# Kernel optimization log

Measured on AMD Instinct MI355X. Metric: run time of the kernel, lower is better.

The kernel has to match this reference:

```python
import jax, jax.numpy as jnp
import numpy as np

B, N, DIN, D, NH, NL = 4, 256, 4, 64, 4, 2
DH = D // NH
EPS = 1e-5
SLOPE = 0.01  # torch LeakyReLU default negative_slope


def setup_inputs() -> dict:
    key = jax.random.key(0)
    ks = jax.random.split(key, 16)
    def p(k, shape, s=0.05):
        return jax.random.normal(k, shape, jnp.float32) * s
    return {
        "feature": jax.random.normal(ks[0], (B, N, N, DIN), jnp.float32),
        "W1": p(ks[1], (DIN, D)), "b1": jnp.zeros((D,), jnp.float32),
        "mw": p(ks[2], (NH, D)), "mb": jnp.zeros((NH,), jnp.float32),
        "bn_gamma": jnp.ones((D,), jnp.float32), "bn_beta": jnp.zeros((D,), jnp.float32),
        "Wq": p(ks[3], (NL, D, D)), "bq": jnp.zeros((NL, D), jnp.float32),
        "Wk": p(ks[4], (NL, D, D)), "bk": jnp.zeros((NL, D), jnp.float32),
        "Wv": p(ks[5], (NL, D, D)), "bv": jnp.zeros((NL, D), jnp.float32),
        "Wo": p(ks[6], (NL, D, D)), "bo": jnp.zeros((NL, D), jnp.float32),
        "ln1_g": jnp.ones((NL, D), jnp.float32), "ln1_b": jnp.zeros((NL, D), jnp.float32),
        "Wff1": p(ks[7], (NL, D, 2 * D)), "bff1": jnp.zeros((NL, 2 * D), jnp.float32),
        "Wff2": p(ks[8], (NL, 2 * D, D)), "bff2": jnp.zeros((NL, D), jnp.float32),
        "ln2_g": jnp.ones((NL, D), jnp.float32), "ln2_b": jnp.zeros((NL, D), jnp.float32),
    }


def _leaky(x):
    return jnp.where(x >= 0, x, SLOPE * x)


def _layer_norm(x, g, b):
    m = x.mean(axis=-1, keepdims=True)
    v = x.var(axis=-1, keepdims=True)
    return g * (x - m) / jnp.sqrt(v + EPS) + b


def reference(feature, W1, b1, mw, mb, bn_gamma, bn_beta,
              Wq, bq, Wk, bk, Wv, bv, Wo, bo, ln1_g, ln1_b,
              Wff1, bff1, Wff2, bff2, ln2_g, ln2_b):
    # linear1: (B,N,N,DIN) -> (B,N,N,D)
    feat = feature @ W1 + b1
    # per-head scalar attention score over node pairs: (NH,B,N,N)
    s = jnp.einsum('bijh,nh->nbij', feat, mw) + mb[:, None, None, None]
    w = jnp.exp(_leaky(s))
    w = w / w.sum(axis=3, keepdims=True)  # softmax-like over second node dim j
    # weighted aggregation: sum over i, then mean over heads -> (B,N,D)
    h = jnp.einsum('nbij,bijh->bjh', w, feat) / NH
    # BatchNorm1d over channels D, stats over (B,N) (training-mode, biased var)
    m = h.mean(axis=(0, 1))
    v = h.var(axis=(0, 1))
    x = bn_gamma * (h - m) / jnp.sqrt(v + EPS) + bn_beta  # (B,N,D)
    # standard post-LN TransformerEncoder, NL layers
    scale = 1.0 / np.sqrt(DH).astype(np.float32)
    for l in range(NL):
        q = (x @ Wq[l] + bq[l]).reshape(B, N, NH, DH)
        k = (x @ Wk[l] + bk[l]).reshape(B, N, NH, DH)
        vv = (x @ Wv[l] + bv[l]).reshape(B, N, NH, DH)
        a = jax.nn.softmax(jnp.einsum('bqhd,bkhd->bhqk', q, k) * scale, axis=-1)
        o = jnp.einsum('bhqk,bkhd->bqhd', a, vv).reshape(B, N, D) @ Wo[l] + bo[l]
        x = _layer_norm(x + o, ln1_g[l], ln1_b[l])
        f = jax.nn.relu(x @ Wff1[l] + bff1[l]) @ Wff2[l] + bff2[l]
        x = _layer_norm(x + f, ln2_g[l], ln2_b[l])
    return x
```

## Files before the change

### kernel.cpp

```cpp
#include <hip/hip_runtime.h>
#include <math.h>

#define B 4
#define N 256
#define DIN 4
#define D 64
#define NH 4
#define NL 2
#define DH 16

constexpr float EPS = 1e-5f;
constexpr float SLOPE = 0.01f;

__global__ void __launch_bounds__(512) k_rowsum(
    const float* __restrict__ feature, const float* __restrict__ W1,
    const float* __restrict__ b1, const float* __restrict__ mw,
    const float* __restrict__ mb, float* __restrict__ rs,
    float* __restrict__ bnacc ) {
    __shared__ float M[16];
    __shared__ float C[4];
    __shared__ float part[32];
    int t = threadIdx.x;
    int lane = t & 63, w = t >> 6;
    int cb = blockIdx.x;
    if (cb == 0 && t < 128) bnacc[t] = 0.f;
    if (t < 16) {
        int n = t >> 2, kk = t & 3;
        float s = 0.f;
        for (int d = 0; d < D; ++d) s += W1[kk * D + d] * mw[n * D + d];
        M[t] = s;
    } else if (t < 20) {
        int n = t - 16;
        float s = mb[n];
        for (int d = 0; d < D; ++d) s += b1[d] * mw[n * D + d];
        C[n] = s;
    }
    __syncthreads();

    int r = w & 3, mh = w >> 2;
    int bi = cb * 4 + r;
    const float4* fb = (const float4*)(feature) + (size_t)bi * N;
    float sn[4] = {0.f, 0.f, 0.f, 0.f};
#pragma unroll
    for (int mm = 0; mm < 2; ++mm) {
        float4 f = fb[lane + 64 * (mh * 2 + mm)];
#pragma unroll
        for (int n = 0; n < 4; ++n) {
            float s = C[n] + f.x * M[n*4+0] + f.y * M[n*4+1] + f.z * M[n*4+2] + f.w * M[n*4+3];
            s = (s >= 0.f) ? s : SLOPE * s;
            sn[n] += __expf(s);
        }
    }
#pragma unroll
    for (int n = 0; n < 4; ++n)
#pragma unroll
        for (int off = 32; off > 0; off >>= 1) sn[n] += __shfl_xor(sn[n], off);
    if (lane == 0) {
#pragma unroll
        for (int n = 0; n < 4; ++n) part[w * 4 + n] = sn[n];
    }
    __syncthreads();
    if (t < 16) {
        int rr = t >> 2, n = t & 3;
        rs[((size_t)(cb * 4 + rr)) * 4 + n] = part[rr * 4 + n] + part[(rr + 4) * 4 + n];
    }
}

__global__ void __launch_bounds__(512) k_aggregate(
    const float* __restrict__ feature, const float* __restrict__ W1,
    const float* __restrict__ b1, const float* __restrict__ mw,
    const float* __restrict__ mb, const float* __restrict__ rs,
    float* __restrict__ h, float* __restrict__ bnacc) {
    __shared__ float M[16];
    __shared__ float C[4];
    __shared__ float part[8][10];
    __shared__ float gacc[20];
    __shared__ float hs[4][D];
    int t = threadIdx.x;
    int lane = t & 63, w = t >> 6;
    int cb = blockIdx.x;
    if (t < 16) {
        int n = t >> 2, kk = t & 3;
        float s = 0.f;
        for (int d = 0; d < D; ++d) s += W1[kk * D + d] * mw[n * D + d];
        M[t] = s;
    } else if (t < 20) {
        int n = t - 16;
        float s = mb[n];
        for (int d = 0; d < D; ++d) s += b1[d] * mw[n * D + d];
        C[n] = s;
    }
    __syncthreads();

    int b = cb >> 6, j0 = (cb & 63) * 4;
    int i = t & 255, jh = t >> 8;
    const float4* fb = (const float4*)(feature) + ((size_t)(b * N + i) * N + j0 + jh * 2);
    float4 f[2];
    f[0] = fb[0];
    f[1] = fb[1];
    float4 r4 = *(const float4*)(rs + (size_t)(b * N + i) * 4);
    float rinv[4] = {1.f / r4.x, 1.f / r4.y, 1.f / r4.z, 1.f / r4.w};
    float acc[2][5];
#pragma unroll
    for (int jj = 0; jj < 2; ++jj) {
        float wbar = 0.f;
#pragma unroll
        for (int n = 0; n < 4; ++n) {
            float s = C[n] + f[jj].x * M[n*4+0] + f[jj].y * M[n*4+1] + f[jj].z * M[n*4+2] + f[jj].w * M[n*4+3];
            s = (s >= 0.f) ? s : SLOPE * s;
            wbar += __expf(s) * rinv[n];
        }
        wbar *= 0.25f;
        acc[jj][0] = wbar * f[jj].x; acc[jj][1] = wbar * f[jj].y;
        acc[jj][2] = wbar * f[jj].z; acc[jj][3] = wbar * f[jj].w;
        acc[jj][4] = wbar;
    }
#pragma unroll
    for (int jj = 0; jj < 2; ++jj)
#pragma unroll
        for (int c = 0; c < 5; ++c)
#pragma unroll
            for (int off = 32; off > 0; off >>= 1) acc[jj][c] += __shfl_xor(acc[jj][c], off);
    if (lane == 0) {
#pragma unroll
        for (int jj = 0; jj < 2; ++jj)
#pragma unroll
            for (int c = 0; c < 5; ++c) part[w][jj * 5 + c] = acc[jj][c];
    }
    __syncthreads();
    if (t < 20) {
        int jj = t / 5, c = t - jj * 5;
        int g = jj >> 1, jjl = jj & 1;
        gacc[t] = part[g*4+0][jjl*5+c] + part[g*4+1][jjl*5+c]
                + part[g*4+2][jjl*5+c] + part[g*4+3][jjl*5+c];
    }
    __syncthreads();
    if (t < 256) {
        float hv = gacc[w * 5 + 4] * b1[lane];
#pragma unroll
        for (int kk = 0; kk < 4; ++kk) hv += gacc[w * 5 + kk] * W1[kk * D + lane];
        h[((size_t)(b * N + j0 + w)) * D + lane] = hv;
        hs[w][lane] = hv;
    }
    __syncthreads();
    if (t < 64) {
        float s = hs[0][lane] + hs[1][lane] + hs[2][lane] + hs[3][lane];
        float sq = hs[0][lane]*hs[0][lane] + hs[1][lane]*hs[1][lane]
                 + hs[2][lane]*hs[2][lane] + hs[3][lane]*hs[3][lane];
        atomicAdd(bnacc + lane, s);
        atomicAdd(bnacc + D + lane, sq);
    }
}

__global__ void __launch_bounds__(256, 4) k_qkv0(
    const float* __restrict__ h, const float* __restrict__ bnacc,
    const float* __restrict__ bn_g, const float* __restrict__ bn_b,
    const float* __restrict__ Wq, const float* __restrict__ bq,
    const float* __restrict__ Wk, const float* __restrict__ bk,
    const float* __restrict__ Wv, const float* __restrict__ bv,
    float* __restrict__ x, float* __restrict__ q,
    float* __restrict__ k, float* __restrict__ v) {
    __shared__ float pp[4][192];
    int t = threadIdx.x, lane = t & 63, w = t >> 6, ch = lane;
    int b = blockIdx.x, n = blockIdx.y;
    int token = b * N + n;
    float mean = bnacc[ch] * (1.0f / (B * N));
    float var = bnacc[D + ch] * (1.0f / (B * N)) - mean * mean;
    float inv = rsqrtf(var + EPS);
    float xv = bn_g[ch] * (h[(size_t)token * D + ch] - mean) * inv + bn_b[ch];
    if (w == 0) x[(size_t)token * D + ch] = xv;
    float aq = 0.f, ak = 0.f, av = 0.f;
#pragma unroll
    for (int i = 0; i < 16; ++i) {
        int kk = w * 16 + i;
        float xx = __shfl(xv, kk);
        aq += xx * Wq[kk * D + ch];
        ak += xx * Wk[kk * D + ch];
        av += xx * Wv[kk * D + ch];
    }
    pp[w][ch] = aq; pp[w][64 + ch] = ak; pp[w][128 + ch] = av;
    __syncthreads();
    if (w < 3) {
        int o = w * 64;
        float val = pp[0][o + ch] + pp[1][o + ch] + pp[2][o + ch] + pp[3][o + ch];
        int head = ch >> 4, dh = ch & (DH - 1);
        size_t oidx = (((size_t)(b * NH + head)) * N + n) * DH + dh;
        if (w == 0) q[oidx] = val + bq[ch];
        else if (w == 1) k[oidx] = val + bk[ch];
        else v[oidx] = val + bv[ch];
    }
}

__global__ void __launch_bounds__(256, 4) k_layer(
    const float* __restrict__ q, const float* __restrict__ k,
    const float* __restrict__ v,
    const float* __restrict__ Wo, const float* __restrict__ bo,
    const float* __restrict__ ln1g, const float* __restrict__ ln1b,
    const float* __restrict__ Wff1, const float* __restrict__ bff1,
    const float* __restrict__ Wff2, const float* __restrict__ bff2,
    const float* __restrict__ ln2g, const float* __restrict__ ln2b,
    const float* __restrict__ Wqn, const float* __restrict__ bqn,
    const float* __restrict__ Wkn, const float* __restrict__ bkn,
    const float* __restrict__ Wvn, const float* __restrict__ bvn,
    float* __restrict__ qo, float* __restrict__ ko, float* __restrict__ vo,
    float* __restrict__ x) {
    __shared__ float attS[D];
    __shared__ float ppA[4][192];
    __shared__ float ppB[4][192];
    int t = threadIdx.x, lane = t & 63, w = t >> 6, ch = lane;
    int b = blockIdx.x, n = blockIdx.y;
    int token = b * N + n;
    size_t xidx = (size_t)token * D + ch;
    float xv = x[xidx];

    int bh = b * NH + w;
    const float* qp = q + ((size_t)bh * N + n) * DH;
    float4 qv[4];
#pragma unroll
    for (int c = 0; c < 4; ++c) qv[c] = ((const float4*)qp)[c];
    const float* kb = k + (size_t)bh * N * DH;
    const float* vb = v + (size_t)bh * N * DH;
    float o[DH];
#pragma unroll
    for (int d = 0; d < DH; ++d) o[d] = 0.f;
    float l = 0.f;
#pragma unroll 2
    for (int cc = 0; cc < 4; ++cc) {
        int key = cc * 64 + lane;
        const float4* kp4 = (const float4*)(kb + (size_t)key * DH);
        const float4* vp4 = (const float4*)(vb + (size_t)key * DH);
        float4 Kc[4], Vc[4];
#pragma unroll
        for (int c = 0; c < 4; ++c) { Kc[c] = kp4[c]; Vc[c] = vp4[c]; }
        float s = 0.f;
#pragma unroll
        for (int c = 0; c < 4; ++c)
            s += qv[c].x * Kc[c].x + qv[c].y * Kc[c].y +
                 qv[c].z * Kc[c].z + qv[c].w * Kc[c].w;
        float p = __expf(s * 0.25f);
        l += p;
#pragma unroll
        for (int c = 0; c < 4; ++c) {
            o[4*c+0] += p * Vc[c].x;
            o[4*c+1] += p * Vc[c].y;
            o[4*c+2] += p * Vc[c].z;
            o[4*c+3] += p * Vc[c].w;
        }
    }
#pragma unroll
    for (int off = 32; off > 0; off >>= 1) l += __shfl_xor(l, off);
#pragma unroll
    for (int d = 0; d < DH; ++d)
#pragma unroll
        for (int off = 32; off > 0; off >>= 1) o[d] += __shfl_xor(o[d], off);
    float rl = 1.f / l;
    if (lane < DH) {
        float sel = o[0];
#pragma unroll
        for (int d = 1; d < DH; ++d) if (lane == d) sel = o[d];
        attS[w * DH + lane] = sel * rl;
    }
    __syncthreads();

    {
        float acc = 0.f;
#pragma unroll
        for (int i = 0; i < 16; ++i) {
            int kk = w * 16 + i;
            acc += attS[kk] * Wo[kk * D + ch];
        }
        ppA[w][ch] = acc;
    }
    __syncthreads();
    float oo = bo[ch] + ppA[0][ch] + ppA[1][ch] + ppA[2][ch] + ppA[3][ch];
    float r = xv + oo;
    float s1 = r, sq1 = r * r;
#pragma unroll
    for (int off = 32; off > 0; off >>= 1) {
        s1 += __shfl_xor(s1, off);
        sq1 += __shfl_xor(sq1, off);
    }
    float mean1 = s1 * (1.0f / D);
    float var1 = sq1 * (1.0f / D) - mean1 * mean1;
    float x1 = ln1g[ch] * (r - mean1) * rsqrtf(var1 + EPS) + ln1b[ch];

    {
        float u = 0.f, g = 0.f;
#pragma unroll
        for (int i = 0; i < 16; ++i) {
            int kk = w * 16 + i;
            float xx = __shfl(x1, kk);
            u += xx * Wff1[kk * 2 * D + ch];
            g += xx * Wff1[kk * 2 * D + D + ch];
        }
        ppB[w][ch] = u; ppB[w][64 + ch] = g;
    }
    __syncthreads();
    float f1lo = fmaxf(bff1[ch] + ppB[0][ch] + ppB[1][ch] + ppB[2][ch] + ppB[3][ch], 0.f);
    float f1hi = fmaxf(bff1[D + ch] + ppB[0][64+ch] + ppB[1][64+ch] + ppB[2][64+ch] + ppB[3][64+ch], 0.f);

    {
        float src = (w < 2) ? f1lo : f1hi;
        int kb0 = (w & 1) * 32;
        float acc = 0.f;
#pragma unroll
        for (int i = 0; i < 32; ++i) {
            int kk = (w >> 1) * 64 + kb0 + i;
            float xx = __shfl(src, kb0 + i);
            acc += xx * Wff2[kk * D + ch];
        }
        ppA[w][ch] = acc;
    }
    __syncthreads();
    float o2 = bff2[ch] + ppA[0][ch] + ppA[1][ch] + ppA[2][ch] + ppA[3][ch];
    float r2 = x1 + o2;
    float s2 = r2, sq2 = r2 * r2;
#pragma unroll
    for (int off = 32; off > 0; off >>= 1) {
        s2 += __shfl_xor(s2, off);
        sq2 += __shfl_xor(sq2, off);
    }
    float mean2 = s2 * (1.0f / D);
    float var2 = sq2 * (1.0f / D) - mean2 * mean2;
    float xnew = ln2g[ch] * (r2 - mean2) * rsqrtf(var2 + EPS) + ln2b[ch];
    if (w == 0) x[xidx] = xnew;

    if (Wqn != nullptr) {
        float aq = 0.f, ak = 0.f, avv = 0.f;
#pragma unroll
        for (int i = 0; i < 16; ++i) {
            int kk = w * 16 + i;
            float xx = __shfl(xnew, kk);
            aq  += xx * Wqn[kk * D + ch];
            ak  += xx * Wkn[kk * D + ch];
            avv += xx * Wvn[kk * D + ch];
        }
        ppB[w][ch] = aq; ppB[w][64 + ch] = ak; ppB[w][128 + ch] = avv;
        __syncthreads();
        if (w < 3) {
            int off = w * 64;
            float val = ppB[0][off+ch] + ppB[1][off+ch] + ppB[2][off+ch] + ppB[3][off+ch];
            int head = ch >> 4, dh = ch & (DH - 1);
            size_t oidx = (((size_t)(b * NH + head)) * N + n) * DH + dh;
            if (w == 0) qo[oidx] = val + bqn[ch];
            else if (w == 1) ko[oidx] = val + bkn[ch];
            else vo[oidx] = val + bvn[ch];
        }
    }
}

extern "C" void kernel_launch(void* const* d_in, const int* in_sizes, int n_in,
                              void* d_out, int out_size, void* d_ws, size_t ws_size,
                              hipStream_t stream) {
    const float* feature = (const float*)d_in[0];
    const float* W1   = (const float*)d_in[1];
    const float* b1   = (const float*)d_in[2];
    const float* mw   = (const float*)d_in[3];
    const float* mb   = (const float*)d_in[4];
    const float* bn_g = (const float*)d_in[5];
    const float* bn_b = (const float*)d_in[6];
    const float* Wq   = (const float*)d_in[7];
    const float* bq   = (const float*)d_in[8];
    const float* Wk   = (const float*)d_in[9];
    const float* bk   = (const float*)d_in[10];
    const float* Wv   = (const float*)d_in[11];
    const float* bv   = (const float*)d_in[12];
    const float* Wo   = (const float*)d_in[13];
    const float* bo   = (const float*)d_in[14];
    const float* ln1g = (const float*)d_in[15];
    const float* ln1b = (const float*)d_in[16];
    const float* Wff1 = (const float*)d_in[17];
    const float* bff1 = (const float*)d_in[18];
    const float* Wff2 = (const float*)d_in[19];
    const float* bff2 = (const float*)d_in[20];
    const float* ln2g = (const float*)d_in[21];
    const float* ln2b = (const float*)d_in[22];

    float* ws    = (float*)d_ws;
    float* rs    = ws;
    float* bnacc = rs + B * N * NH;
    float* h     = bnacc + 128;
    float* q     = h + B * N * D;
    float* k0    = q + B * N * D;
    float* v0    = k0 + B * N * D;
    float* k1    = v0 + B * N * D;
    float* v1    = k1 + B * N * D;
    float* x     = (float*)d_out;

    k_rowsum<<<256, 512, 0, stream>>>(feature, W1, b1, mw, mb, rs, bnacc);
    k_aggregate<<<256, 512, 0, stream>>>(feature, W1, b1, mw, mb, rs, h, bnacc);
    k_qkv0<<<dim3(B, N), 256, 0, stream>>>(h, bnacc, bn_g, bn_b,
                                           Wq, bq, Wk, bk, Wv, bv, x, q, k0, v0);
    k_layer<<<dim3(B, N), 256, 0, stream>>>(q, k0, v0,
        Wo, bo, ln1g, ln1b, Wff1, bff1, Wff2, bff2, ln2g, ln2b,
        Wq + (size_t)D * D, bq + D, Wk + (size_t)D * D, bk + D,
        Wv + (size_t)D * D, bv + D, q, k1, v1, x);
    k_layer<<<dim3(B, N), 256, 0, stream>>>(q, k1, v1,
        Wo + (size_t)D * D, bo + D, ln1g + D, ln1b + D,
        Wff1 + (size_t)D * 2 * D, bff1 + 2 * D,
        Wff2 + (size_t)2 * D * D, bff2 + D, ln2g + D, ln2b + D,
        nullptr, nullptr, nullptr, nullptr, nullptr, nullptr,
        nullptr, nullptr, nullptr, x);
}
```

Measured before the change: 153.0 us.

## Process two tokens per block in layer kernels and prefetch weights to registers

The QKV and transformer-layer kernels now handle two tokens per block, halving the grid. Each weight value loaded into registers is reused for both tokens, and weight loads are issued ahead of the barriers so their latency can overlap with the preceding reductions. The M/C projection in the rowsum and aggregate kernels is recomputed per wave with shuffle reductions, replacing the serial 16-thread loop and its barrier. In exchange the kernels use more registers and shared memory, which may lower occupancy, and the smaller grid exposes less parallelism.

```diff
diff --git a/kernel.cpp b/kernel.cpp
--- a/kernel.cpp
+++ b/kernel.cpp
@@ -12,41 +12,60 @@
 constexpr float EPS = 1e-5f;
 constexpr float SLOPE = 0.01f;
 
+__device__ __forceinline__ void mc_proj(
+    const float* __restrict__ W1, const float* __restrict__ b1,
+    const float* __restrict__ mw, const float* __restrict__ mb,
+    int lane, float* Mreg , float* Creg ) {
+    float w1v[4];
+#pragma unroll
+    for (int kk = 0; kk < 4; ++kk) w1v[kk] = W1[kk * D + lane];
+    float b1v = b1[lane];
+#pragma unroll
+    for (int n = 0; n < 4; ++n) {
+        float mwv = mw[n * D + lane];
+        float p0 = w1v[0] * mwv, p1 = w1v[1] * mwv;
+        float p2 = w1v[2] * mwv, p3 = w1v[3] * mwv;
+        float pc = b1v * mwv;
+#pragma unroll
+        for (int off = 32; off > 0; off >>= 1) {
+            p0 += __shfl_xor(p0, off); p1 += __shfl_xor(p1, off);
+            p2 += __shfl_xor(p2, off); p3 += __shfl_xor(p3, off);
+            pc += __shfl_xor(pc, off);
+        }
+        Mreg[n * 4 + 0] = p0; Mreg[n * 4 + 1] = p1;
+        Mreg[n * 4 + 2] = p2; Mreg[n * 4 + 3] = p3;
+        Creg[n] = pc + mb[n];
+    }
+}
+
 __global__ void __launch_bounds__(512) k_rowsum(
     const float* __restrict__ feature, const float* __restrict__ W1,
     const float* __restrict__ b1, const float* __restrict__ mw,
     const float* __restrict__ mb, float* __restrict__ rs,
     float* __restrict__ bnacc ) {
-    __shared__ float M[16];
-    __shared__ float C[4];
     __shared__ float part[32];
     int t = threadIdx.x;
     int lane = t & 63, w = t >> 6;
     int cb = blockIdx.x;
     if (cb == 0 && t < 128) bnacc[t] = 0.f;
-    if (t < 16) {
-        int n = t >> 2, kk = t & 3;
-        float s = 0.f;
-        for (int d = 0; d < D; ++d) s += W1[kk * D + d] * mw[n * D + d];
-        M[t] = s;
-    } else if (t < 20) {
-        int n = t - 16;
-        float s = mb[n];
-        for (int d = 0; d < D; ++d) s += b1[d] * mw[n * D + d];
-        C[n] = s;
-    }
-    __syncthreads();
 
     int r = w & 3, mh = w >> 2;
     int bi = cb * 4 + r;
     const float4* fb = (const float4*)(feature) + (size_t)bi * N;
+    float4 f0 = fb[lane + 64 * (mh * 2 + 0)];
+    float4 f1 = fb[lane + 64 * (mh * 2 + 1)];
+
+    float Mreg[16], Creg[4];
+    mc_proj(W1, b1, mw, mb, lane, Mreg, Creg);
+
     float sn[4] = {0.f, 0.f, 0.f, 0.f};
 #pragma unroll
     for (int mm = 0; mm < 2; ++mm) {
-        float4 f = fb[lane + 64 * (mh * 2 + mm)];
+        float4 f = (mm == 0) ? f0 : f1;
 #pragma unroll
         for (int n = 0; n < 4; ++n) {
-            float s = C[n] + f.x * M[n*4+0] + f.y * M[n*4+1] + f.z * M[n*4+2] + f.w * M[n*4+3];
+            float s = Creg[n] + f.x * Mreg[n*4+0] + f.y * Mreg[n*4+1]
+                              + f.z * Mreg[n*4+2] + f.w * Mreg[n*4+3];
             s = (s >= 0.f) ? s : SLOPE * s;
             sn[n] += __expf(s);
         }
@@ -71,26 +90,12 @@
     const float* __restrict__ b1, const float* __restrict__ mw,
     const float* __restrict__ mb, const float* __restrict__ rs,
     float* __restrict__ h, float* __restrict__ bnacc) {
-    __shared__ float M[16];
-    __shared__ float C[4];
     __shared__ float part[8][10];
     __shared__ float gacc[20];
     __shared__ float hs[4][D];
     int t = threadIdx.x;
     int lane = t & 63, w = t >> 6;
     int cb = blockIdx.x;
-    if (t < 16) {
-        int n = t >> 2, kk = t & 3;
-        float s = 0.f;
-        for (int d = 0; d < D; ++d) s += W1[kk * D + d] * mw[n * D + d];
-        M[t] = s;
-    } else if (t < 20) {
-        int n = t - 16;
-        float s = mb[n];
-        for (int d = 0; d < D; ++d) s += b1[d] * mw[n * D + d];
-        C[n] = s;
-    }
-    __syncthreads();
 
     int b = cb >> 6, j0 = (cb & 63) * 4;
     int i = t & 255, jh = t >> 8;
@@ -99,6 +104,14 @@
     f[0] = fb[0];
     f[1] = fb[1];
     float4 r4 = *(const float4*)(rs + (size_t)(b * N + i) * 4);
+
+    float Mreg[16], Creg[4];
+    mc_proj(W1, b1, mw, mb, lane, Mreg, Creg);
+    float w1v[4];
+#pragma unroll
+    for (int kk = 0; kk < 4; ++kk) w1v[kk] = W1[kk * D + lane];
+    float b1v = b1[lane];
+
     float rinv[4] = {1.f / r4.x, 1.f / r4.y, 1.f / r4.z, 1.f / r4.w};
     float acc[2][5];
 #pragma unroll
@@ -106,7 +119,8 @@
         float wbar = 0.f;
 #pragma unroll
         for (int n = 0; n < 4; ++n) {
-            float s = C[n] + f[jj].x * M[n*4+0] + f[jj].y * M[n*4+1] + f[jj].z * M[n*4+2] + f[jj].w * M[n*4+3];
+            float s = Creg[n] + f[jj].x * Mreg[n*4+0] + f[jj].y * Mreg[n*4+1]
+                              + f[jj].z * Mreg[n*4+2] + f[jj].w * Mreg[n*4+3];
             s = (s >= 0.f) ? s : SLOPE * s;
             wbar += __expf(s) * rinv[n];
         }
@@ -136,9 +150,9 @@
     }
     __syncthreads();
     if (t < 256) {
-        float hv = gacc[w * 5 + 4] * b1[lane];
-#pragma unroll
-        for (int kk = 0; kk < 4; ++kk) hv += gacc[w * 5 + kk] * W1[kk * D + lane];
+        float hv = gacc[w * 5 + 4] * b1v;
+#pragma unroll
+        for (int kk = 0; kk < 4; ++kk) hv += gacc[w * 5 + kk] * w1v[kk];
         h[((size_t)(b * N + j0 + w)) * D + lane] = hv;
         hs[w][lane] = hv;
     }
@@ -160,37 +174,55 @@
     const float* __restrict__ Wv, const float* __restrict__ bv,
     float* __restrict__ x, float* __restrict__ q,
     float* __restrict__ k, float* __restrict__ v) {
-    __shared__ float pp[4][192];
+    __shared__ float xs[2][D];
+    __shared__ float pp[4][2][192];
     int t = threadIdx.x, lane = t & 63, w = t >> 6, ch = lane;
-    int b = blockIdx.x, n = blockIdx.y;
-    int token = b * N + n;
+    int b = blockIdx.x, n0 = blockIdx.y * 2;
+
+    float wq[16], wk[16], wv[16];
+#pragma unroll
+    for (int i = 0; i < 16; ++i) {
+        int kk = w * 16 + i;
+        wq[i] = Wq[kk * D + ch];
+        wk[i] = Wk[kk * D + ch];
+        wv[i] = Wv[kk * D + ch];
+    }
     float mean = bnacc[ch] * (1.0f / (B * N));
     float var = bnacc[D + ch] * (1.0f / (B * N)) - mean * mean;
     float inv = rsqrtf(var + EPS);
-    float xv = bn_g[ch] * (h[(size_t)token * D + ch] - mean) * inv + bn_b[ch];
-    if (w == 0) x[(size_t)token * D + ch] = xv;
-    float aq = 0.f, ak = 0.f, av = 0.f;
+    size_t xi0 = ((size_t)(b * N + n0)) * D + ch;
+    float xv0 = bn_g[ch] * (h[xi0] - mean) * inv + bn_b[ch];
+    float xv1 = bn_g[ch] * (h[xi0 + D] - mean) * inv + bn_b[ch];
+    if (w == 0) { x[xi0] = xv0; xs[0][ch] = xv0; }
+    if (w == 1) { x[xi0 + D] = xv1; xs[1][ch] = xv1; }
+    __syncthreads();
+
+    float aq0=0.f, ak0=0.f, av0=0.f, aq1=0.f, ak1=0.f, av1=0.f;
 #pragma unroll
     for (int i = 0; i < 16; ++i) {
         int kk = w * 16 + i;
-        float xx = __shfl(xv, kk);
-        aq += xx * Wq[kk * D + ch];
-        ak += xx * Wk[kk * D + ch];
-        av += xx * Wv[kk * D + ch];
-    }
-    pp[w][ch] = aq; pp[w][64 + ch] = ak; pp[w][128 + ch] = av;
+        float xx0 = xs[0][kk], xx1 = xs[1][kk];
+        aq0 += xx0 * wq[i]; ak0 += xx0 * wk[i]; av0 += xx0 * wv[i];
+        aq1 += xx1 * wq[i]; ak1 += xx1 * wk[i]; av1 += xx1 * wv[i];
+    }
+    pp[w][0][ch] = aq0; pp[w][0][64 + ch] = ak0; pp[w][0][128 + ch] = av0;
+    pp[w][1][ch] = aq1; pp[w][1][64 + ch] = ak1; pp[w][1][128 + ch] = av1;
     __syncthreads();
     if (w < 3) {
         int o = w * 64;
-        float val = pp[0][o + ch] + pp[1][o + ch] + pp[2][o + ch] + pp[3][o + ch];
         int head = ch >> 4, dh = ch & (DH - 1);
-        size_t oidx = (((size_t)(b * NH + head)) * N + n) * DH + dh;
-        if (w == 0) q[oidx] = val + bq[ch];
-        else if (w == 1) k[oidx] = val + bk[ch];
-        else v[oidx] = val + bv[ch];
+#pragma unroll
+        for (int tk = 0; tk < 2; ++tk) {
+            float val = pp[0][tk][o+ch] + pp[1][tk][o+ch] + pp[2][tk][o+ch] + pp[3][tk][o+ch];
+            size_t oidx = (((size_t)(b * NH + head)) * N + (n0 + tk)) * DH + dh;
+            if (w == 0) q[oidx] = val + bq[ch];
+            else if (w == 1) k[oidx] = val + bk[ch];
+            else v[oidx] = val + bv[ch];
+        }
     }
 }
 
+template <bool FUSE>
 __global__ void __launch_bounds__(256, 4) k_layer(
     const float* __restrict__ q, const float* __restrict__ k,
     const float* __restrict__ v,
@@ -204,27 +236,33 @@
     const float* __restrict__ Wvn, const float* __restrict__ bvn,
     float* __restrict__ qo, float* __restrict__ ko, float* __restrict__ vo,
     float* __restrict__ x) {
-    __shared__ float attS[D];
-    __shared__ float ppA[4][192];
-    __shared__ float ppB[4][192];
+    __shared__ float attS[2][D];
+    __shared__ float xs[2][D];
+    __shared__ float f1s[2][2 * D];
+    __shared__ float ppA[4][2][192];
+    __shared__ float ppB[4][2][192];
     int t = threadIdx.x, lane = t & 63, w = t >> 6, ch = lane;
-    int b = blockIdx.x, n = blockIdx.y;
-    int token = b * N + n;
-    size_t xidx = (size_t)token * D + ch;
-    float xv = x[xidx];
+    int b = blockIdx.x, n0 = blockIdx.y * 2;
+
+    size_t xi0 = ((size_t)(b * N + n0)) * D + ch;
+    float xv0 = x[xi0], xv1 = x[xi0 + D];
+    float bo_r = bo[ch], l1g = ln1g[ch], l1b = ln1b[ch];
+    float bf1a = bff1[ch], bf1b = bff1[D + ch];
+    float bf2_r = bff2[ch], l2g = ln2g[ch], l2b = ln2b[ch];
 
     int bh = b * NH + w;
-    const float* qp = q + ((size_t)bh * N + n) * DH;
-    float4 qv[4];
-#pragma unroll
-    for (int c = 0; c < 4; ++c) qv[c] = ((const float4*)qp)[c];
+    const float4* qp0 = (const float4*)(q + ((size_t)bh * N + n0) * DH);
+    const float4* qp1 = (const float4*)(q + ((size_t)bh * N + n0 + 1) * DH);
+    float4 qv0[4], qv1[4];
+#pragma unroll
+    for (int c = 0; c < 4; ++c) { qv0[c] = qp0[c]; qv1[c] = qp1[c]; }
     const float* kb = k + (size_t)bh * N * DH;
     const float* vb = v + (size_t)bh * N * DH;
-    float o[DH];
-#pragma unroll
-    for (int d = 0; d < DH; ++d) o[d] = 0.f;
-    float l = 0.f;
-#pragma unroll 2
+    float o0[DH], o1[DH];
+#pragma unroll
+    for (int d = 0; d < DH; ++d) { o0[d] = 0.f; o1[d] = 0.f; }
+    float l0 = 0.f, l1 = 0.f;
+#pragma unroll 1
     for (int cc = 0; cc < 4; ++cc) {
         int key = cc * 64 + lane;
         const float4* kp4 = (const float4*)(kb + (size_t)key * DH);
@@ -232,119 +270,181 @@
         float4 Kc[4], Vc[4];
 #pragma unroll
         for (int c = 0; c < 4; ++c) { Kc[c] = kp4[c]; Vc[c] = vp4[c]; }
-        float s = 0.f;
-#pragma unroll
-        for (int c = 0; c < 4; ++c)
-            s += qv[c].x * Kc[c].x + qv[c].y * Kc[c].y +
-                 qv[c].z * Kc[c].z + qv[c].w * Kc[c].w;
-        float p = __expf(s * 0.25f);
-        l += p;
+        float s0 = 0.f, s1 = 0.f;
 #pragma unroll
         for (int c = 0; c < 4; ++c) {
-            o[4*c+0] += p * Vc[c].x;
-            o[4*c+1] += p * Vc[c].y;
-            o[4*c+2] += p * Vc[c].z;
-            o[4*c+3] += p * Vc[c].w;
-        }
-    }
-#pragma unroll
-    for (int off = 32; off > 0; off >>= 1) l += __shfl_xor(l, off);
-#pragma unroll
-    for (int d = 0; d < DH; ++d)
-#pragma unroll
-        for (int off = 32; off > 0; off >>= 1) o[d] += __shfl_xor(o[d], off);
-    float rl = 1.f / l;
+            s0 += qv0[c].x * Kc[c].x + qv0[c].y * Kc[c].y +
+                  qv0[c].z * Kc[c].z + qv0[c].w * Kc[c].w;
+            s1 += qv1[c].x * Kc[c].x + qv1[c].y * Kc[c].y +
+                  qv1[c].z * Kc[c].z + qv1[c].w * Kc[c].w;
+        }
+        float p0 = __expf(s0 * 0.25f);
+        float p1 = __expf(s1 * 0.25f);
+        l0 += p0; l1 += p1;
+#pragma unroll
+        for (int c = 0; c < 4; ++c) {
+            o0[4*c+0] += p0 * Vc[c].x; o0[4*c+1] += p0 * Vc[c].y;
+            o0[4*c+2] += p0 * Vc[c].z; o0[4*c+3] += p0 * Vc[c].w;
+            o1[4*c+0] += p1 * Vc[c].x; o1[4*c+1] += p1 * Vc[c].y;
+            o1[4*c+2] += p1 * Vc[c].z; o1[4*c+3] += p1 * Vc[c].w;
+        }
+    }
+    float wo[16];
+#pragma unroll
+    for (int i = 0; i < 16; ++i) wo[i] = Wo[(w * 16 + i) * D + ch];
+
+#pragma unroll
+    for (int off = 32; off > 0; off >>= 1) {
+        l0 += __shfl_xor(l0, off);
+        l1 += __shfl_xor(l1, off);
+    }
+#pragma unroll
+    for (int d = 0; d < DH; ++d) {
+#pragma unroll
+        for (int off = 32; off > 0; off >>= 1) {
+            o0[d] += __shfl_xor(o0[d], off);
+            o1[d] += __shfl_xor(o1[d], off);
+        }
+    }
+    float rl0 = 1.f / l0, rl1 = 1.f / l1;
     if (lane < DH) {
-        float sel = o[0];
-#pragma unroll
-        for (int d = 1; d < DH; ++d) if (lane == d) sel = o[d];
-        attS[w * DH + lane] = sel * rl;
+        float sel0 = o0[0], sel1 = o1[0];
+#pragma unroll
+        for (int d = 1; d < DH; ++d)
+            if (lane == d) { sel0 = o0[d]; sel1 = o1[d]; }
+        attS[0][w * DH + lane] = sel0 * rl0;
+        attS[1][w * DH + lane] = sel1 * rl1;
     }
     __syncthreads();
 
     {
-        float acc = 0.f;
+        float a0 = 0.f, a1 = 0.f;
 #pragma unroll
         for (int i = 0; i < 16; ++i) {
             int kk = w * 16 + i;
-            acc += attS[kk] * Wo[kk * D + ch];
-        }
-        ppA[w][ch] = acc;
-    }
-    __syncthreads();
-    float oo = bo[ch] + ppA[0][ch] + ppA[1][ch] + ppA[2][ch] + ppA[3][ch];
-    float r = xv + oo;
-    float s1 = r, sq1 = r * r;
+            float wv = wo[i];
+            a0 += attS[0][kk] * wv;
+            a1 += attS[1][kk] * wv;
+        }
+        ppA[w][0][ch] = a0; ppA[w][1][ch] = a1;
+    }
+    float wf1a[16], wf1b[16];
+#pragma unroll
+    for (int i = 0; i < 16; ++i) {
+        int kk = w * 16 + i;
+        wf1a[i] = Wff1[kk * 2 * D + ch];
+        wf1b[i] = Wff1[kk * 2 * D + D + ch];
+    }
+    __syncthreads();
+
+    float r0 = xv0 + bo_r + ppA[0][0][ch] + ppA[1][0][ch] + ppA[2][0][ch] + ppA[3][0][ch];
+    float r1 = xv1 + bo_r + ppA[0][1][ch] + ppA[1][1][ch] + ppA[2][1][ch] + ppA[3][1][ch];
+    float s0a = r0, q0a = r0 * r0, s1a = r1, q1a = r1 * r1;
 #pragma unroll
     for (int off = 32; off > 0; off >>= 1) {
-        s1 += __shfl_xor(s1, off);
-        sq1 += __shfl_xor(sq1, off);
-    }
-    float mean1 = s1 * (1.0f / D);
-    float var1 = sq1 * (1.0f / D) - mean1 * mean1;
-    float x1 = ln1g[ch] * (r - mean1) * rsqrtf(var1 + EPS) + ln1b[ch];
+        s0a += __shfl_xor(s0a, off); q0a += __shfl_xor(q0a, off);
+        s1a += __shfl_xor(s1a, off); q1a += __shfl_xor(q1a, off);
+    }
+    float mean10 = s0a * (1.0f / D), var10 = q0a * (1.0f / D) - mean10 * mean10;
+    float mean11 = s1a * (1.0f / D), var11 = q1a * (1.0f / D) - mean11 * mean11;
+    float x1_0 = l1g * (r0 - mean10) * rsqrtf(var10 + EPS) + l1b;
+    float x1_1 = l1g * (r1 - mean11) * rsqrtf(var11 + EPS) + l1b;
+    if (w == 0) xs[0][ch] = x1_0;
+    if (w == 1) xs[1][ch] = x1_1;
+    __syncthreads();
 
     {
-        float u = 0.f, g = 0.f;
+        float u0=0.f, g0=0.f, u1=0.f, g1=0.f;
 #pragma unroll
         for (int i = 0; i < 16; ++i) {
             int kk = w * 16 + i;
-            float xx = __shfl(x1, kk);
-            u += xx * Wff1[kk * 2 * D + ch];
-            g += xx * Wff1[kk * 2 * D + D + ch];
-        }
-        ppB[w][ch] = u; ppB[w][64 + ch] = g;
-    }
-    __syncthreads();
-    float f1lo = fmaxf(bff1[ch] + ppB[0][ch] + ppB[1][ch] + ppB[2][ch] + ppB[3][ch], 0.f);
-    float f1hi = fmaxf(bff1[D + ch] + ppB[0][64+ch] + ppB[1][64+ch] + ppB[2][64+ch] + ppB[3][64+ch], 0.f);
+            float xx0 = xs[0][kk], xx1 = xs[1][kk];
+            u0 += xx0 * wf1a[i]; g0 += xx0 * wf1b[i];
+            u1 += xx1 * wf1a[i]; g1 += xx1 * wf1b[i];
+        }
+        ppB[w][0][ch] = u0; ppB[w][0][64 + ch] = g0;
+        ppB[w][1][ch] = u1; ppB[w][1][64 + ch] = g1;
+    }
+    float wf2[32];
+#pragma unroll
+    for (int i = 0; i < 32; ++i) wf2[i] = Wff2[(w * 32 + i) * D + ch];
+    __syncthreads();
 
     {
-        float src = (w < 2) ? f1lo : f1hi;
-        int kb0 = (w & 1) * 32;
-        float acc = 0.f;
+        float a00 = fmaxf(bf1a + ppB[0][0][ch] + ppB[1][0][ch] + ppB[2][0][ch] + ppB[3][0][ch], 0.f);
+        float a01 = fmaxf(bf1b + ppB[0][0][64+ch] + ppB[1][0][64+ch] + ppB[2][0][64+ch] + ppB[3][0][64+ch], 0.f);
+        float a10 = fmaxf(bf1a + ppB[0][1][ch] + ppB[1][1][ch] + ppB[2][1][ch] + ppB[3][1][ch], 0.f);
+        float a11 = fmaxf(bf1b + ppB[0][1][64+ch] + ppB[1][1][64+ch] + ppB[2][1][64+ch] + ppB[3][1][64+ch], 0.f);
+        if (w == 0) { f1s[0][ch] = a00; f1s[0][64 + ch] = a01; }
+        if (w == 1) { f1s[1][ch] = a10; f1s[1][64 + ch] = a11; }
+    }
+    __syncthreads();
+
+    {
+        float e0 = 0.f, e1 = 0.f;
 #pragma unroll
         for (int i = 0; i < 32; ++i) {
-            int kk = (w >> 1) * 64 + kb0 + i;
-            float xx = __shfl(src, kb0 + i);
-            acc += xx * Wff2[kk * D + ch];
-        }
-        ppA[w][ch] = acc;
-    }
-    __syncthreads();
-    float o2 = bff2[ch] + ppA[0][ch] + ppA[1][ch] + ppA[2][ch] + ppA[3][ch];
-    float r2 = x1 + o2;
-    float s2 = r2, sq2 = r2 * r2;
-#pragma unroll
-    for (int off = 32; off > 0; off >>= 1) {
-        s2 += __shfl_xor(s2, off);
-        sq2 += __shfl_xor(sq2, off);
-    }
-    float mean2 = s2 * (1.0f / D);
-    float var2 = sq2 * (1.0f / D) - mean2 * mean2;
-    float xnew = ln2g[ch] * (r2 - mean2) * rsqrtf(var2 + EPS) + ln2b[ch];
-    if (w == 0) x[xidx] = xnew;
-
-    if (Wqn != nullptr) {
-        float aq = 0.f, ak = 0.f, avv = 0.f;
+            int kk = w * 32 + i;
+            float xx0 = f1s[0][kk], xx1 = f1s[1][kk];
+            e0 += xx0 * wf2[i];
+            e1 += xx1 * wf2[i];
+        }
+        ppA[w][0][ch] = e0; ppA[w][1][ch] = e1;
+    }
+    float wqn[16], wkn[16], wvn[16];
+    if (FUSE) {
 #pragma unroll
         for (int i = 0; i < 16; ++i) {
             int kk = w * 16 + i;
-            float xx = __shfl(xnew, kk);
-            aq  += xx * Wqn[kk * D + ch];
-            ak  += xx * Wkn[kk * D + ch];
-            avv += xx * Wvn[kk * D + ch];
-        }
-        ppB[w][ch] = aq; ppB[w][64 + ch] = ak; ppB[w][128 + ch] = avv;
+            wqn[i] = Wqn[kk * D + ch];
+            wkn[i] = Wkn[kk * D + ch];
+            wvn[i] = Wvn[kk * D + ch];
+        }
+    }
+    __syncthreads();
+
+    float o2_0 = bf2_r + ppA[0][0][ch] + ppA[1][0][ch] + ppA[2][0][ch] + ppA[3][0][ch];
+    float o2_1 = bf2_r + ppA[0][1][ch] + ppA[1][1][ch] + ppA[2][1][ch] + ppA[3][1][ch];
+    float r20 = x1_0 + o2_0, r21 = x1_1 + o2_1;
+    float s0b = r20, q0b = r20 * r20, s1b = r21, q1b = r21 * r21;
+#pragma unroll
+    for (int off = 32; off > 0; off >>= 1) {
+        s0b += __shfl_xor(s0b, off); q0b += __shfl_xor(q0b, off);
+        s1b += __shfl_xor(s1b, off); q1b += __shfl_xor(q1b, off);
+    }
+    float mean20 = s0b * (1.0f / D), var20 = q0b * (1.0f / D) - mean20 * mean20;
+    float mean21 = s1b * (1.0f / D), var21 = q1b * (1.0f / D) - mean21 * mean21;
+    float xn0 = l2g * (r20 - mean20) * rsqrtf(var20 + EPS) + l2b;
+    float xn1 = l2g * (r21 - mean21) * rsqrtf(var21 + EPS) + l2b;
+    if (w == 0) x[xi0] = xn0;
+    if (w == 1) x[xi0 + D] = xn1;
+
+    if (FUSE) {
+        if (w == 0) xs[0][ch] = xn0;
+        if (w == 1) xs[1][ch] = xn1;
+        __syncthreads();
+        float aq0=0.f, ak0=0.f, av0=0.f, aq1=0.f, ak1=0.f, av1=0.f;
+#pragma unroll
+        for (int i = 0; i < 16; ++i) {
+            int kk = w * 16 + i;
+            float xx0 = xs[0][kk], xx1 = xs[1][kk];
+            aq0 += xx0 * wqn[i]; ak0 += xx0 * wkn[i]; av0 += xx0 * wvn[i];
+            aq1 += xx1 * wqn[i]; ak1 += xx1 * wkn[i]; av1 += xx1 * wvn[i];
+        }
+        ppB[w][0][ch] = aq0; ppB[w][0][64 + ch] = ak0; ppB[w][0][128 + ch] = av0;
+        ppB[w][1][ch] = aq1; ppB[w][1][64 + ch] = ak1; ppB[w][1][128 + ch] = av1;
         __syncthreads();
         if (w < 3) {
-            int off = w * 64;
-            float val = ppB[0][off+ch] + ppB[1][off+ch] + ppB[2][off+ch] + ppB[3][off+ch];
+            int o = w * 64;
             int head = ch >> 4, dh = ch & (DH - 1);
-            size_t oidx = (((size_t)(b * NH + head)) * N + n) * DH + dh;
-            if (w == 0) qo[oidx] = val + bqn[ch];
-            else if (w == 1) ko[oidx] = val + bkn[ch];
-            else vo[oidx] = val + bvn[ch];
+#pragma unroll
+            for (int tk = 0; tk < 2; ++tk) {
+                float val = ppB[0][tk][o+ch] + ppB[1][tk][o+ch] + ppB[2][tk][o+ch] + ppB[3][tk][o+ch];
+                size_t oidx = (((size_t)(b * NH + head)) * N + (n0 + tk)) * DH + dh;
+                if (w == 0) qo[oidx] = val + bqn[ch];
+                else if (w == 1) ko[oidx] = val + bkn[ch];
+                else vo[oidx] = val + bvn[ch];
+            }
         }
     }
 }
@@ -389,13 +489,13 @@
 
     k_rowsum<<<256, 512, 0, stream>>>(feature, W1, b1, mw, mb, rs, bnacc);
     k_aggregate<<<256, 512, 0, stream>>>(feature, W1, b1, mw, mb, rs, h, bnacc);
-    k_qkv0<<<dim3(B, N), 256, 0, stream>>>(h, bnacc, bn_g, bn_b,
-                                           Wq, bq, Wk, bk, Wv, bv, x, q, k0, v0);
-    k_layer<<<dim3(B, N), 256, 0, stream>>>(q, k0, v0,
+    k_qkv0<<<dim3(B, N / 2), 256, 0, stream>>>(h, bnacc, bn_g, bn_b,
+                                               Wq, bq, Wk, bk, Wv, bv, x, q, k0, v0);
+    k_layer<true><<<dim3(B, N / 2), 256, 0, stream>>>(q, k0, v0,
         Wo, bo, ln1g, ln1b, Wff1, bff1, Wff2, bff2, ln2g, ln2b,
         Wq + (size_t)D * D, bq + D, Wk + (size_t)D * D, bk + D,
         Wv + (size_t)D * D, bv + D, q, k1, v1, x);
-    k_layer<<<dim3(B, N), 256, 0, stream>>>(q, k1, v1,
+    k_layer<false><<<dim3(B, N / 2), 256, 0, stream>>>(q, k1, v1,
         Wo + (size_t)D * D, bo + D, ln1g + D, ln1b + D,
         Wff1 + (size_t)D * 2 * D, bff1 + 2 * D,
         Wff2 + (size_t)2 * D * D, bff2 + D, ln2g + D, ln2b + D,
```

Result: faster. 147.7 us (-3.4%).
